# Optimization experiments

Hardware: AMD Instinct MI355X
Metric: run time of the kernel (lower is better)

## Reference

```python
import jax, jax.numpy as jnp
import numpy as np

N, IN_DIM, HID, OUT = 8192, 512, 256, 64
NEG_INF = -9e15


def setup_inputs() -> dict:
    key = jax.random.key(0)
    ks = jax.random.split(key, 7)
    X = jax.random.normal(ks[0], (N, IN_DIM), dtype=jnp.float32)
    A = jax.random.randint(ks[1], (N, N), 0, 2, dtype=jnp.int32)
    # fc1 (Linear): kaiming-uniform-ish init, exact dist irrelevant for correctness
    W1 = jax.random.normal(ks[2], (IN_DIM, HID), dtype=jnp.float32) / np.sqrt(IN_DIM)
    b1 = jnp.zeros((HID,), dtype=jnp.float32)
    # attention vector a: xavier_uniform(gain=1.414) on shape (2*HID, 1)
    lim = 1.414 * np.sqrt(6.0 / (2 * HID + 1))
    a = jax.random.uniform(ks[3], (2 * HID, 1), minval=-lim, maxval=lim, dtype=jnp.float32)
    Omega = jax.random.normal(ks[4], (HID, OUT), dtype=jnp.float32) * np.sqrt(2.0 / (HID + OUT))
    beta = jnp.zeros((OUT,), dtype=jnp.float32)
    return {"X": X, "A": A, "W1": W1, "b1": b1, "a": a, "Omega": Omega, "beta": beta}


def reference(X, A, W1, b1, a, Omega, beta):
    H1 = X @ W1 + b1                      # [N, HID]
    # score(i,j) = leakyrelu(a[:HID].H1_i + a[HID:].H1_j) -- computed via broadcast,
    # avoiding the O(N^2 * 2*HID) concat the torch code materializes.
    a1 = a[:HID, 0]                       # [HID]
    a2 = a[HID:, 0]                       # [HID]
    e = jax.nn.leaky_relu((H1 @ a1)[:, None] + (H1 @ a2)[None, :], negative_slope=0.2)  # [N, N]
    e = jnp.where(A > 0, e, NEG_INF)
    attention = jax.nn.softmax(e, axis=1)  # dropout_rate=0.0 -> identity
    H2 = attention @ H1                    # [N, HID]
    return jax.nn.sigmoid(H2 @ Omega + beta)  # [N, OUT]
```

## Files before the change

### kernel.cpp

```cpp
#include <hip/hip_runtime.h>
#include <hip/hip_bf16.h>


typedef float f32x4 __attribute__((ext_vector_type(4)));
typedef short s16x8 __attribute__((ext_vector_type(8)));

#define NN 8192
#define INDIM 512
#define HIDD 256
#define OUTD 64

static __device__ __forceinline__ short f2bf(float x) {
    __hip_bfloat16 h = __float2bfloat16(x);
    return __builtin_bit_cast(short, h);
}

static __device__ __forceinline__ void split_bf(float x, short& hi, short& lo) {
    short h = f2bf(x);
    unsigned int hb = ((unsigned int)(unsigned short)h) << 16;
    float hf = __builtin_bit_cast(float, hb);
    hi = h;
    lo = f2bf(x - hf);
}

__global__ void k_splitW1(const float* __restrict__ W1,
                          short* __restrict__ W1Thi, short* __restrict__ W1Tlo) {
    int t = blockIdx.x * 256 + threadIdx.x;
    int n = t >> 9;
    int k = t & 511;
    float x = W1[k * 256 + n];
    short hi, lo; split_bf(x, hi, lo);
    W1Thi[t] = hi;
    W1Tlo[t] = lo;
}

__global__ void __launch_bounds__(256, 2)
k_h1(const float* __restrict__ X, const short* __restrict__ W1Thi,
     const short* __restrict__ W1Tlo, const float* __restrict__ b1,
     const float* __restrict__ avec, unsigned short* __restrict__ H1TB,
     float* __restrict__ alw, float* __restrict__ bew, float* __restrict__ uvw) {
    __shared__ float s1p[4][16];
    __shared__ float s2p[4][16];
    const int tid = threadIdx.x;
    const int wn = tid >> 6, lane = tid & 63;
    const int q = lane >> 4, m16 = lane & 15;
    const int i0 = blockIdx.x * 16;
    const int irow = i0 + m16;

    f32x4 zero4 = {0.f, 0.f, 0.f, 0.f};
    f32x4 acc[4];
#pragma unroll
    for (int nt = 0; nt < 4; ++nt) acc[nt] = zero4;

    const float* Xrow = X + (size_t)irow * INDIM;
    for (int kk = 0; kk < INDIM; kk += 32) {
        const int k0 = kk + q * 8;
        float4 xa = *(const float4*)(Xrow + k0);
        float4 xb = *(const float4*)(Xrow + k0 + 4);
        float xs[8] = {xa.x, xa.y, xa.z, xa.w, xb.x, xb.y, xb.z, xb.w};
        s16x8 ahi, alo;
#pragma unroll
        for (int j = 0; j < 8; ++j) { short h, l; split_bf(xs[j], h, l); ahi[j] = h; alo[j] = l; }
#pragma unroll
        for (int nt = 0; nt < 4; ++nt) {
            const int n = wn * 64 + nt * 16 + m16;
            s16x8 bhi = *(const s16x8*)(W1Thi + n * INDIM + k0);
            s16x8 blo = *(const s16x8*)(W1Tlo + n * INDIM + k0);
            acc[nt] = __builtin_amdgcn_mfma_f32_16x16x32_bf16(ahi, bhi, acc[nt], 0, 0, 0);
            acc[nt] = __builtin_amdgcn_mfma_f32_16x16x32_bf16(ahi, blo, acc[nt], 0, 0, 0);
            acc[nt] = __builtin_amdgcn_mfma_f32_16x16x32_bf16(alo, bhi, acc[nt], 0, 0, 0);
        }
    }

    float p1[4] = {0.f, 0.f, 0.f, 0.f};
    float p2[4] = {0.f, 0.f, 0.f, 0.f};
    const int rowbase = i0 + q * 4;
    const int chunk = rowbase >> 5, win = rowbase & 31;
#pragma unroll
    for (int nt = 0; nt < 4; ++nt) {
        const int col = wn * 64 + nt * 16 + m16;
        const float b1v = b1[col];
        const float a1v = avec[col];
        const float a2v = avec[HIDD + col];
        float v0 = acc[nt][0] + b1v;
        float v1 = acc[nt][1] + b1v;
        float v2 = acc[nt][2] + b1v;
        float v3 = acc[nt][3] + b1v;
        ushort4 us;
        us.x = (unsigned short)f2bf(v0);
        us.y = (unsigned short)f2bf(v1);
        us.z = (unsigned short)f2bf(v2);
        us.w = (unsigned short)f2bf(v3);
        *(ushort4*)(H1TB + (size_t)chunk * 8192 + col * 32 + win) = us;
        p1[0] += v0 * a1v; p1[1] += v1 * a1v; p1[2] += v2 * a1v; p1[3] += v3 * a1v;
        p2[0] += v0 * a2v; p2[1] += v1 * a2v; p2[2] += v2 * a2v; p2[3] += v3 * a2v;
    }
#pragma unroll
    for (int off = 1; off < 16; off <<= 1) {
#pragma unroll
        for (int r = 0; r < 4; ++r) {
            p1[r] += __shfl_xor(p1[r], off);
            p2[r] += __shfl_xor(p2[r], off);
        }
    }
    if (m16 == 0) {
#pragma unroll
        for (int r = 0; r < 4; ++r) {
            s1p[wn][q * 4 + r] = p1[r];
            s2p[wn][q * 4 + r] = p2[r];
        }
    }
    __syncthreads();
    if (tid < 16) {
        const int i = i0 + tid;
        float s1 = s1p[0][tid] + s1p[1][tid] + s1p[2][tid] + s1p[3][tid];
        float s2 = s2p[0][tid] + s2p[1][tid] + s2p[2][tid] + s2p[3][tid];
        alw[i] = expf(s1);
        bew[i] = expf(0.2f * s1);
        uvw[2 * i]     = expf(s2);
        uvw[2 * i + 1] = expf(0.2f * s2);
    }
}

__global__ void __launch_bounds__(256, 4)
k_attn(const int* __restrict__ A, const unsigned short* __restrict__ H1TB,
       const float* __restrict__ alw, const float* __restrict__ bew,
       const float* __restrict__ uvw,
       float* __restrict__ H2acc, float* __restrict__ Zw) {
    __shared__ unsigned short tile[2][8192];

    const int tid = threadIdx.x;
    const int wave = tid >> 6, lane = tid & 63;
    const int q = lane >> 4, m16 = lane & 15;
    const int wm = wave & 1, wn = wave >> 1;
    const int mb = blockIdx.x & 255;
    const int ks = blockIdx.x >> 8;
    const int i = mb * 32 + wm * 16 + m16;
    const float al = alw[i], be = bew[i];

    const unsigned short* gp = H1TB + (size_t)ks * 64 * 8192 + tid * 8;
    __attribute__((address_space(3))) unsigned short* tl =
        (__attribute__((address_space(3))) unsigned short*)&tile[0][0];

    const int* Ap = A + (size_t)i * NN + ks * 2048 + q * 8;
    const float* uvp = uvw + 2 * (ks * 2048 + q * 8);

    f32x4 zero4 = {0.f, 0.f, 0.f, 0.f};
    f32x4 acc[8];
#pragma unroll
    for (int nt = 0; nt < 8; ++nt) acc[nt] = zero4;
    float zacc = 0.f;

#pragma unroll
    for (int c = 0; c < 4; ++c)
        __builtin_amdgcn_global_load_lds(
            (const __attribute__((address_space(1))) void*)(gp + c * 2048),
            (__attribute__((address_space(3))) void*)(tl + c * 2048 + tid * 8),
            16, 0, 0);
    gp += 8192;

    int4 A0 = *(const int4*)(Ap);
    int4 A1 = *(const int4*)(Ap + 4);
    float4 uv0 = *(const float4*)(uvp);
    float4 uv1 = *(const float4*)(uvp + 4);
    float4 uv2 = *(const float4*)(uvp + 8);
    float4 uv3 = *(const float4*)(uvp + 12);
    Ap += 32; uvp += 64;

    for (int kk = 0; kk < 64; ++kk) {
        float wv[8];
        wv[0] = (A0.x > 0) ? fmaxf(al * uv0.x, be * uv0.y) : 0.f;
        wv[1] = (A0.y > 0) ? fmaxf(al * uv0.z, be * uv0.w) : 0.f;
        wv[2] = (A0.z > 0) ? fmaxf(al * uv1.x, be * uv1.y) : 0.f;
        wv[3] = (A0.w > 0) ? fmaxf(al * uv1.z, be * uv1.w) : 0.f;
        wv[4] = (A1.x > 0) ? fmaxf(al * uv2.x, be * uv2.y) : 0.f;
        wv[5] = (A1.y > 0) ? fmaxf(al * uv2.z, be * uv2.w) : 0.f;
        wv[6] = (A1.z > 0) ? fmaxf(al * uv3.x, be * uv3.y) : 0.f;
        wv[7] = (A1.w > 0) ? fmaxf(al * uv3.z, be * uv3.w) : 0.f;
        zacc += (wv[0] + wv[1] + wv[2] + wv[3]) + (wv[4] + wv[5] + wv[6] + wv[7]);
        s16x8 af;
#pragma unroll
        for (int j = 0; j < 8; ++j) af[j] = f2bf(wv[j]);

        __builtin_amdgcn_sched_barrier(0);
        asm volatile("s_waitcnt vmcnt(0)" ::: "memory");
        __builtin_amdgcn_s_barrier();
        __builtin_amdgcn_sched_barrier(0);

        if (kk < 63) {
            A0 = *(const int4*)(Ap);
            A1 = *(const int4*)(Ap + 4);
            uv0 = *(const float4*)(uvp);
            uv1 = *(const float4*)(uvp + 4);
            uv2 = *(const float4*)(uvp + 8);
            uv3 = *(const float4*)(uvp + 12);
            Ap += 32; uvp += 64;
            const int nb = ((kk + 1) & 1) * 8192;
#pragma unroll
            for (int c = 0; c < 4; ++c)
                __builtin_amdgcn_global_load_lds(
                    (const __attribute__((address_space(1))) void*)(gp + c * 2048),
                    (__attribute__((address_space(3))) void*)(tl + nb + c * 2048 + tid * 8),
                    16, 0, 0);
            gp += 8192;
        }

        const unsigned short* tb = &tile[kk & 1][0];
#pragma unroll
        for (int nt = 0; nt < 8; ++nt) {
            s16x8 bfv = *(const s16x8*)(tb + (wn * 128 + nt * 16 + m16) * 32 + q * 8);
            acc[nt] = __builtin_amdgcn_mfma_f32_16x16x32_bf16(af, bfv, acc[nt], 0, 0, 0);
        }
    }

    zacc += __shfl_xor(zacc, 16);
    zacc += __shfl_xor(zacc, 32);
    if (wn == 0 && q == 0) atomicAdd(&Zw[i], zacc);

    const int rowbase = mb * 32 + wm * 16 + q * 4;
#pragma unroll
    for (int nt = 0; nt < 8; ++nt) {
        const int col = wn * 128 + nt * 16 + m16;
#pragma unroll
        for (int r = 0; r < 4; ++r)
            atomicAdd(&H2acc[(size_t)(rowbase + r) * HIDD + col], acc[nt][r]);
    }
}

__global__ void __launch_bounds__(256)
k_out(const float* __restrict__ H2acc, const float* __restrict__ Zw,
      const float* __restrict__ Omega, const float* __restrict__ beta,
      float* __restrict__ out) {
    __shared__ float om[HIDD * OUTD];
    const int tid = threadIdx.x;
    for (int idx = tid; idx < HIDD * OUTD; idx += 256) om[idx] = Omega[idx];
    __syncthreads();
    const int wave = tid >> 6, o = tid & 63;
    const float bv = beta[o];
    for (int rr = 0; rr < 8; ++rr) {
        const int i = blockIdx.x * 32 + wave * 8 + rr;
        const float4* H2v = (const float4*)(H2acc + (size_t)i * HIDD);
        float acc = 0.f;
#pragma unroll 4
        for (int c4 = 0; c4 < 64; ++c4) {
            float4 h = H2v[c4];
            const int cb = c4 * 4;
            acc = fmaf(h.x, om[(cb + 0) * OUTD + o], acc);
            acc = fmaf(h.y, om[(cb + 1) * OUTD + o], acc);
            acc = fmaf(h.z, om[(cb + 2) * OUTD + o], acc);
            acc = fmaf(h.w, om[(cb + 3) * OUTD + o], acc);
        }
        const float zinv = 1.0f / Zw[i];
        const float logit = acc * zinv + bv;
        out[(size_t)i * OUTD + o] = 1.0f / (1.0f + expf(-logit));
    }
}

extern "C" void kernel_launch(void* const* d_in, const int* in_sizes, int n_in,
                              void* d_out, int out_size, void* d_ws, size_t ws_size,
                              hipStream_t stream) {
    const float* X     = (const float*)d_in[0];
    const int*   A     = (const int*)d_in[1];
    const float* W1    = (const float*)d_in[2];
    const float* b1    = (const float*)d_in[3];
    const float* avec  = (const float*)d_in[4];
    const float* Omega = (const float*)d_in[5];
    const float* beta  = (const float*)d_in[6];
    float* out = (float*)d_out;

    char* ws = (char*)d_ws;
    unsigned short* H1TB = (unsigned short*)(ws + 0);
    short* W1Thi = (short*)(ws + 4194304);
    short* W1Tlo = (short*)(ws + 4456448);
    float* alw   = (float*)(ws + 4718592);
    float* bew   = (float*)(ws + 4751360);
    float* uvw   = (float*)(ws + 4784128);
    float* Zw    = (float*)(ws + 4849664);
    float* H2acc = (float*)(ws + 4882432);

    hipMemsetAsync(Zw, 0, 32768 + 8388608, stream);

    k_splitW1<<<512, 256, 0, stream>>>(W1, W1Thi, W1Tlo);
    k_h1<<<512, 256, 0, stream>>>(X, W1Thi, W1Tlo, b1, avec, H1TB, alw, bew, uvw);
    k_attn<<<1024, 256, 0, stream>>>(A, H1TB, alw, bew, uvw, H2acc, Zw);
    k_out<<<256, 256, 0, stream>>>(H2acc, Zw, Omega, beta, out);
}
```

Before: 562.0 us.

## Bit-pack the adjacency mask in a pre-pass and read bits in attention kernel

Adds a k_packA kernel that streams the int32 adjacency matrix once and packs each 8-element group into one byte, laid out so each attention lane gets 32 bits covering four k-steps. The attention kernel then loads one 32-bit word per four iterations instead of two int4 loads per iteration. The wait is relaxed to vmcnt(1) so the prefetched mask word can stay in flight. The full A read still happens, now in a separate streaming pass plus an extra kernel launch. In exchange, the attention main loop carries far less global traffic and fewer registers for A.

```diff
diff --git a/kernel.cpp b/kernel.cpp
--- a/kernel.cpp
+++ b/kernel.cpp
@@ -21,6 +21,33 @@
     float hf = __builtin_bit_cast(float, hb);
     hi = h;
     lo = f2bf(x - hf);
+}
+
+__global__ void __launch_bounds__(256)
+k_packA(const int* __restrict__ A, unsigned int* __restrict__ Apk) {
+    const int i = blockIdx.x;
+    const int t = threadIdx.x;
+    const int ks = t >> 6, q = (t >> 4) & 3, kk0 = t & 15;
+    const int* Ar = A + (size_t)i * NN;
+    unsigned int out = 0;
+#pragma unroll
+    for (int kkq = 0; kkq < 4; ++kkq) {
+        const int kk = kk0 * 4 + kkq;
+        const int c0 = ks * 2048 + kk * 32 + q * 8;
+        int4 v0 = *(const int4*)(Ar + c0);
+        int4 v1 = *(const int4*)(Ar + c0 + 4);
+        unsigned int b = 0;
+        b |= (v0.x > 0) ? 1u : 0u;
+        b |= (v0.y > 0) ? 2u : 0u;
+        b |= (v0.z > 0) ? 4u : 0u;
+        b |= (v0.w > 0) ? 8u : 0u;
+        b |= (v1.x > 0) ? 16u : 0u;
+        b |= (v1.y > 0) ? 32u : 0u;
+        b |= (v1.z > 0) ? 64u : 0u;
+        b |= (v1.w > 0) ? 128u : 0u;
+        out |= b << (kkq * 8);
+    }
+    Apk[(size_t)i * 256 + t] = out;
 }
 
 __global__ void k_splitW1(const float* __restrict__ W1,
@@ -123,7 +150,7 @@
 }
 
 __global__ void __launch_bounds__(256, 4)
-k_attn(const int* __restrict__ A, const unsigned short* __restrict__ H1TB,
+k_attn(const unsigned int* __restrict__ Apk, const unsigned short* __restrict__ H1TB,
        const float* __restrict__ alw, const float* __restrict__ bew,
        const float* __restrict__ uvw,
        float* __restrict__ H2acc, float* __restrict__ Zw) {
@@ -142,7 +169,7 @@
     __attribute__((address_space(3))) unsigned short* tl =
         (__attribute__((address_space(3))) unsigned short*)&tile[0][0];
 
-    const int* Ap = A + (size_t)i * NN + ks * 2048 + q * 8;
+    const unsigned int* Ab = Apk + (size_t)i * 256 + ks * 64 + q * 16;
     const float* uvp = uvw + 2 * (ks * 2048 + q * 8);
 
     f32x4 zero4 = {0.f, 0.f, 0.f, 0.f};
@@ -159,58 +186,64 @@
             16, 0, 0);
     gp += 8192;
 
-    int4 A0 = *(const int4*)(Ap);
-    int4 A1 = *(const int4*)(Ap + 4);
     float4 uv0 = *(const float4*)(uvp);
     float4 uv1 = *(const float4*)(uvp + 4);
     float4 uv2 = *(const float4*)(uvp + 8);
     float4 uv3 = *(const float4*)(uvp + 12);
-    Ap += 32; uvp += 64;
-
-    for (int kk = 0; kk < 64; ++kk) {
-        float wv[8];
-        wv[0] = (A0.x > 0) ? fmaxf(al * uv0.x, be * uv0.y) : 0.f;
-        wv[1] = (A0.y > 0) ? fmaxf(al * uv0.z, be * uv0.w) : 0.f;
-        wv[2] = (A0.z > 0) ? fmaxf(al * uv1.x, be * uv1.y) : 0.f;
-        wv[3] = (A0.w > 0) ? fmaxf(al * uv1.z, be * uv1.w) : 0.f;
-        wv[4] = (A1.x > 0) ? fmaxf(al * uv2.x, be * uv2.y) : 0.f;
-        wv[5] = (A1.y > 0) ? fmaxf(al * uv2.z, be * uv2.w) : 0.f;
-        wv[6] = (A1.z > 0) ? fmaxf(al * uv3.x, be * uv3.y) : 0.f;
-        wv[7] = (A1.w > 0) ? fmaxf(al * uv3.z, be * uv3.w) : 0.f;
-        zacc += (wv[0] + wv[1] + wv[2] + wv[3]) + (wv[4] + wv[5] + wv[6] + wv[7]);
-        s16x8 af;
-#pragma unroll
-        for (int j = 0; j < 8; ++j) af[j] = f2bf(wv[j]);
-
-        __builtin_amdgcn_sched_barrier(0);
-        asm volatile("s_waitcnt vmcnt(0)" ::: "memory");
-        __builtin_amdgcn_s_barrier();
-        __builtin_amdgcn_sched_barrier(0);
-
-        if (kk < 63) {
-            A0 = *(const int4*)(Ap);
-            A1 = *(const int4*)(Ap + 4);
-            uv0 = *(const float4*)(uvp);
-            uv1 = *(const float4*)(uvp + 4);
-            uv2 = *(const float4*)(uvp + 8);
-            uv3 = *(const float4*)(uvp + 12);
-            Ap += 32; uvp += 64;
-            const int nb = ((kk + 1) & 1) * 8192;
-#pragma unroll
-            for (int c = 0; c < 4; ++c)
-                __builtin_amdgcn_global_load_lds(
-                    (const __attribute__((address_space(1))) void*)(gp + c * 2048),
-                    (__attribute__((address_space(3))) void*)(tl + nb + c * 2048 + tid * 8),
-                    16, 0, 0);
-            gp += 8192;
-        }
-
-        const unsigned short* tb = &tile[kk & 1][0];
-#pragma unroll
-        for (int nt = 0; nt < 8; ++nt) {
-            s16x8 bfv = *(const s16x8*)(tb + (wn * 128 + nt * 16 + m16) * 32 + q * 8);
-            acc[nt] = __builtin_amdgcn_mfma_f32_16x16x32_bf16(af, bfv, acc[nt], 0, 0, 0);
-        }
+    uvp += 64;
+    unsigned int a4 = Ab[0];
+
+    for (int kk4 = 0; kk4 < 16; ++kk4) {
+        unsigned int a4n = Ab[(kk4 + 1) & 15];
+#pragma unroll
+        for (int kkq = 0; kkq < 4; ++kkq) {
+            const int kk = kk4 * 4 + kkq;
+            const unsigned int ab = a4 >> (kkq * 8);
+
+            float wv[8];
+            wv[0] = (ab & 1u)   ? fmaxf(al * uv0.x, be * uv0.y) : 0.f;
+            wv[1] = (ab & 2u)   ? fmaxf(al * uv0.z, be * uv0.w) : 0.f;
+            wv[2] = (ab & 4u)   ? fmaxf(al * uv1.x, be * uv1.y) : 0.f;
+            wv[3] = (ab & 8u)   ? fmaxf(al * uv1.z, be * uv1.w) : 0.f;
+            wv[4] = (ab & 16u)  ? fmaxf(al * uv2.x, be * uv2.y) : 0.f;
+            wv[5] = (ab & 32u)  ? fmaxf(al * uv2.z, be * uv2.w) : 0.f;
+            wv[6] = (ab & 64u)  ? fmaxf(al * uv3.x, be * uv3.y) : 0.f;
+            wv[7] = (ab & 128u) ? fmaxf(al * uv3.z, be * uv3.w) : 0.f;
+            zacc += (wv[0] + wv[1] + wv[2] + wv[3]) + (wv[4] + wv[5] + wv[6] + wv[7]);
+            s16x8 af;
+#pragma unroll
+            for (int j = 0; j < 8; ++j) af[j] = f2bf(wv[j]);
+
+            __builtin_amdgcn_sched_barrier(0);
+            if (kkq == 0) asm volatile("s_waitcnt vmcnt(1)" ::: "memory");
+            else          asm volatile("s_waitcnt vmcnt(0)" ::: "memory");
+            __builtin_amdgcn_s_barrier();
+            __builtin_amdgcn_sched_barrier(0);
+
+            if (kk < 63) {
+                uv0 = *(const float4*)(uvp);
+                uv1 = *(const float4*)(uvp + 4);
+                uv2 = *(const float4*)(uvp + 8);
+                uv3 = *(const float4*)(uvp + 12);
+                uvp += 64;
+                const int nb = ((kk + 1) & 1) * 8192;
+#pragma unroll
+                for (int c = 0; c < 4; ++c)
+                    __builtin_amdgcn_global_load_lds(
+                        (const __attribute__((address_space(1))) void*)(gp + c * 2048),
+                        (__attribute__((address_space(3))) void*)(tl + nb + c * 2048 + tid * 8),
+                        16, 0, 0);
+                gp += 8192;
+            }
+
+            const unsigned short* tb = &tile[kk & 1][0];
+#pragma unroll
+            for (int nt = 0; nt < 8; ++nt) {
+                s16x8 bfv = *(const s16x8*)(tb + (wn * 128 + nt * 16 + m16) * 32 + q * 8);
+                acc[nt] = __builtin_amdgcn_mfma_f32_16x16x32_bf16(af, bfv, acc[nt], 0, 0, 0);
+            }
+        }
+        a4 = a4n;
     }
 
     zacc += __shfl_xor(zacc, 16);
@@ -277,11 +310,13 @@
     float* uvw   = (float*)(ws + 4784128);
     float* Zw    = (float*)(ws + 4849664);
     float* H2acc = (float*)(ws + 4882432);
+    unsigned int* Apk = (unsigned int*)(ws + 13271040);
 
     hipMemsetAsync(Zw, 0, 32768 + 8388608, stream);
 
+    k_packA<<<8192, 256, 0, stream>>>(A, Apk);
     k_splitW1<<<512, 256, 0, stream>>>(W1, W1Thi, W1Tlo);
     k_h1<<<512, 256, 0, stream>>>(X, W1Thi, W1Tlo, b1, avec, H1TB, alw, bew, uvw);
-    k_attn<<<1024, 256, 0, stream>>>(A, H1TB, alw, bew, uvw, H2acc, Zw);
+    k_attn<<<1024, 256, 0, stream>>>(Apk, H1TB, alw, bew, uvw, H2acc, Zw);
     k_out<<<256, 256, 0, stream>>>(H2acc, Zw, Omega, beta, out);
 }
```

Result: faster. 544.7 us (-3.1%).
